# Performance work log

Hardware: AMD Instinct MI355X
Metric: run time of the kernel (lower is better)

The kernel has to match this reference:

```python
import jax, jax.numpy as jnp
import numpy as np

NUM_EMBEDDINGS = 8192
EMBEDDING_DIM = 64
COMMITMENT_COST = 0.25


def setup_inputs() -> dict:
    key = jax.random.key(0)
    k1, k2 = jax.random.split(key)
    hidden_states = jax.random.normal(k1, (32, 32, 32, EMBEDDING_DIM), dtype=jnp.float32)
    init_bound = 1.0 / NUM_EMBEDDINGS
    embedding = jax.random.uniform(k2, (NUM_EMBEDDINGS, EMBEDDING_DIM), dtype=jnp.float32,
                                   minval=-init_bound, maxval=init_bound)
    return {"hidden_states": hidden_states, "embedding": embedding}


def reference(hidden_states, embedding):
    # hidden_states: (B, H, W, D); embedding: (K, D)
    flat = hidden_states.reshape(-1, EMBEDDING_DIM)            # (N, D)
    z_sq = jnp.sum(flat * flat, axis=1, keepdims=True)          # (N, 1)
    e_sq = jnp.sum(embedding * embedding, axis=1)               # (K,)
    # squared L2 distances: ||z||^2 + ||e||^2 - 2 z.e
    distances = z_sq + e_sq - 2.0 * (flat @ embedding.T)        # (N, K)
    encoding_indices = jnp.argmin(distances, axis=1)            # (N,)
    # one-hot @ embedding == gather; identical math, efficient form
    quantized = jnp.take(embedding, encoding_indices, axis=0).reshape(hidden_states.shape)
    # codebook + commitment loss (return_loss=True path)
    loss = (jnp.mean((jax.lax.stop_gradient(quantized) - hidden_states) ** 2)
            + COMMITMENT_COST * jnp.mean((quantized - jax.lax.stop_gradient(hidden_states)) ** 2))
    # straight-through estimator
    z_q = hidden_states + jax.lax.stop_gradient(quantized - hidden_states)
    B = hidden_states.shape[0]
    min_encoding_indices = encoding_indices.reshape(B, -1)      # (B, num_tokens)
    return z_q, min_encoding_indices, loss
```

## Files before the change

kernel.cpp:

```cpp
#include <hip/hip_runtime.h>
#include <cfloat>

#define N_TOK   32768
#define DIM     64
#define K_CODES 8192
#define NCHK    64
#define TPB     128

#define IDX_OFF  (N_TOK * DIM)
#define LOSS_OFF (N_TOK * DIM + N_TOK)

#define WS_ESQ   0
#define WS_EHIT  8192
#define WS_PART  270336

#define MRG   2e-5f
#define DINIT 6e-5f

typedef __attribute__((ext_vector_type(8)))  short bf16x8;
typedef __attribute__((ext_vector_type(16))) float f32x16;

__device__ inline ushort f2bf(float x) {
    unsigned u = __float_as_uint(x);
    return (ushort)((u + 0x7FFFu + ((u >> 16) & 1u)) >> 16);
}
__device__ inline float bf2f(ushort h) { return __uint_as_float(((unsigned)h) << 16); }
__device__ inline ushort f2bf_up(float x) {
    unsigned u = __float_as_uint(x);
    return (x >= 0.0f) ? (ushort)((u + 0xFFFFu) >> 16) : (ushort)(u >> 16);
}
__device__ inline unsigned long long packdi(float d, int i) {
    unsigned u = __float_as_uint(d);
    u ^= (u & 0x80000000u) ? 0xFFFFFFFFu : 0x80000000u;
    return ((unsigned long long)u << 32) | (unsigned)i;
}

__global__ __launch_bounds__(256) void esq_kernel(const float* __restrict__ emb,
                                                  float* __restrict__ esq) {
#pragma clang fp contract(off)
    const int tid = threadIdx.x;
    const int q = tid & 7;
    const int code = blockIdx.x * 32 + (tid >> 3);
    const float* row = emb + code * DIM;
    float x = row[q];
    float r = x * x;
#pragma unroll
    for (int m = 1; m < 8; ++m) {
        float y = row[q + 8 * m];
        float sq = y * y;
        r = r + sq;
    }
    r = r + __shfl_xor(r, 1, 64);
    r = r + __shfl_xor(r, 2, 64);
    r = r + __shfl_xor(r, 4, 64);
    if (q == 0) esq[code] = r;
}

__global__ __launch_bounds__(256) void pack2(const float* __restrict__ emb,
                                             ushort* __restrict__ ehiT,
                                             float* __restrict__ eT) {
#pragma clang fp contract(off)
    const int k = blockIdx.x * 256 + threadIdx.x;
    float v[64];
    {
        const float4* ep = (const float4*)(emb + (size_t)k * DIM);
#pragma unroll
        for (int i = 0; i < 16; ++i) {
            const float4 a = ep[i];
            v[4 * i] = a.x; v[4 * i + 1] = a.y; v[4 * i + 2] = a.z; v[4 * i + 3] = a.w;
        }
    }
#pragma unroll
    for (int j = 0; j < 64; ++j) eT[(size_t)j * K_CODES + k] = v[j];
    const int sc = k >> 7, lc = k & 127;
#pragma unroll
    for (int q = 0; q < 4; ++q)
#pragma unroll
        for (int h = 0; h < 2; ++h) {
            bf16x8 o;
#pragma unroll
            for (int e = 0; e < 8; ++e) o[e] = (short)f2bf(v[16 * q + 8 * h + e]);
            *(bf16x8*)(ehiT + ((((size_t)sc * 4 + q) * 2 + h) * 128 + lc) * 8) = o;
        }
}

__global__ __launch_bounds__(256, 2) void vq_mfma(const float* __restrict__ hid,
                                                  const ushort* __restrict__ ehiT,
                                                  ushort* __restrict__ Mm) {
#pragma clang fp contract(off)
    const int tid = threadIdx.x;
    const int lane = tid & 63;
    const int w = tid >> 6;
    const int h = lane >> 5;
    const int t0 = blockIdx.x * 64;

    bf16x8 z_hi[2][4];
#pragma unroll
    for (int ts = 0; ts < 2; ++ts)
#pragma unroll
    for (int q = 0; q < 4; ++q) {
        const float* zp = hid + (size_t)(t0 + 32 * ts + (lane & 31)) * DIM + 16 * q + 8 * h;
        const float4 u0 = *(const float4*)zp;
        const float4 u1 = *(const float4*)(zp + 4);
        const float zz[8] = {u0.x, u0.y, u0.z, u0.w, u1.x, u1.y, u1.z, u1.w};
        bf16x8 hv;
#pragma unroll
        for (int i = 0; i < 8; ++i) hv[i] = (short)f2bf(zz[i]);
        z_hi[ts][q] = hv;
    }

    f32x16 zc;
#pragma unroll
    for (int i = 0; i < 16; ++i) zc[i] = 0.0f;

#define ALOAD(SC, R, Q) (*(const bf16x8*)(ehiT + \
    ((((size_t)(SC) * 4 + (Q)) * 2 + h) * 128 + 32 * (R) + (lane & 31)) * 8))

    bf16x8 Aa[4][4], Ab[4][4];
#pragma unroll
    for (int r = 0; r < 4; ++r)
#pragma unroll
        for (int q = 0; q < 4; ++q) Aa[r][q] = ALOAD(w, r, q);

#define MFMA_G(CUR, NXT, G) { \
    const int sc = 4 * (G) + w; \
    const int scn = ((G) + 1 < 16) ? (4 * ((G) + 1) + w) : sc; \
    _Pragma("unroll") \
    for (int r = 0; r < 4; ++r) \
        _Pragma("unroll") \
        for (int q = 0; q < 4; ++q) NXT[r][q] = ALOAD(scn, r, q); \
    float wm0 = -3.0e38f, wm1 = -3.0e38f; \
    _Pragma("unroll") \
    for (int r = 0; r < 4; ++r) { \
        f32x16 d0 = __builtin_amdgcn_mfma_f32_32x32x16_bf16(CUR[r][0], z_hi[0][0], zc, 0, 0, 0); \
        f32x16 d1 = __builtin_amdgcn_mfma_f32_32x32x16_bf16(CUR[r][0], z_hi[1][0], zc, 0, 0, 0); \
        _Pragma("unroll") \
        for (int q = 1; q < 4; ++q) { \
            d0 = __builtin_amdgcn_mfma_f32_32x32x16_bf16(CUR[r][q], z_hi[0][q], d0, 0, 0, 0); \
            d1 = __builtin_amdgcn_mfma_f32_32x32x16_bf16(CUR[r][q], z_hi[1][q], d1, 0, 0, 0); \
        } \
        _Pragma("unroll") \
        for (int i = 0; i < 16; ++i) { \
            wm0 = fmaxf(wm0, d0[i]); \
            wm1 = fmaxf(wm1, d1[i]); \
        } \
    } \
    wm0 = fmaxf(wm0, __shfl_xor(wm0, 32, 64)); \
    wm1 = fmaxf(wm1, __shfl_xor(wm1, 32, 64)); \
    if (lane < 32) { \
        Mm[(size_t)sc * N_TOK + t0 + lane]      = f2bf_up(wm0); \
        Mm[(size_t)sc * N_TOK + t0 + 32 + lane] = f2bf_up(wm1); \
    } }

    for (int gg = 0; gg < 16; gg += 2) {
        MFMA_G(Aa, Ab, gg)
        MFMA_G(Ab, Aa, gg + 1)
    }
#undef MFMA_G
#undef ALOAD
}

__global__ __launch_bounds__(512, 1) void vq_select(const float* __restrict__ hid,
                                                    const float* __restrict__ eT,
                                                    const float* __restrict__ esq,
                                                    const ushort* __restrict__ Mm,
                                                    float* __restrict__ out_idx) {
#pragma clang fp contract(off)
    __shared__ float z_s[TPB][68];
    __shared__ float zsq_s[TPB];
    __shared__ float eps_s[TPB];
    __shared__ float bD_s[TPB];
    __shared__ float mxw[4][TPB];
    __shared__ unsigned long long key_s[TPB];
    __shared__ unsigned long long m0_s[NCHK];
    __shared__ unsigned long long m1_s[NCHK];

    const int tid = threadIdx.x;
    const int lane = tid & 63;
    const int w = tid >> 6;
    const int t0 = blockIdx.x * TPB;

    {
        const int t = tid >> 2;
        const int j4 = (tid & 3) * 4;
        const float4* src = (const float4*)(hid + (size_t)(t0 + t) * DIM);
        float4* dst = (float4*)(&z_s[t][0]);
#pragma unroll
        for (int i = 0; i < 4; ++i) dst[j4 + i] = src[j4 + i];
    }
    if (tid < TPB) key_s[tid] = ~0ull;
    __syncthreads();

    {
        const int token = tid & 127;
        const int cg = tid >> 7;
        float pm = bf2f(Mm[(size_t)(16 * cg) * N_TOK + t0 + token]);
#pragma unroll 5
        for (int c = 16 * cg + 1; c < 16 * cg + 16; ++c)
            pm = fmaxf(pm, bf2f(Mm[(size_t)c * N_TOK + t0 + token]));
        mxw[cg][token] = pm;
    }
    if (tid < TPB) {
        const float* zr = &z_s[tid][0];
        float r[8];
#pragma unroll
        for (int q = 0; q < 8; ++q) {
            float x = zr[q]; r[q] = x * x;
#pragma unroll
            for (int m = 1; m < 8; ++m) {
                float y = zr[q + 8 * m];
                float sq = y * y;
                r[q] = r[q] + sq;
            }
        }
        zsq_s[tid] = ((r[0] + r[1]) + (r[2] + r[3])) + ((r[4] + r[5]) + (r[6] + r[7]));
    }
    __syncthreads();
    if (tid < TPB) {
        const float mx = fmaxf(fmaxf(mxw[0][tid], mxw[1][tid]),
                               fmaxf(mxw[2][tid], mxw[3][tid]));
        const float zsq = zsq_s[tid];
        const float eps = sqrtf(zsq) * 4.2e-6f + 2e-7f;
        eps_s[tid] = eps;
        bD_s[tid] = zsq - 2.0f * mx + 2.0f * eps + DINIT;
    }
    __syncthreads();

#pragma unroll
    for (int i = 0; i < 8; ++i) {
        const int c = 8 * w + i;
        const float mA = bf2f(Mm[(size_t)c * N_TOK + t0 + lane]);
        const int sA = (fmaf(-2.0f, mA + eps_s[lane], zsq_s[lane]) - MRG) < bD_s[lane];
        const unsigned long long b0 = __ballot(sA);
        const float mB = bf2f(Mm[(size_t)c * N_TOK + t0 + 64 + lane]);
        const int sB = (fmaf(-2.0f, mB + eps_s[64 + lane], zsq_s[64 + lane]) - MRG) < bD_s[64 + lane];
        const unsigned long long b1 = __ballot(sB);
        if (lane == 0) { m0_s[c] = b0; m1_s[c] = b1; }
    }

    for (int i = 0; i < 8; ++i) {
        const int c = 8 * w + i;
        unsigned long long msk0 = m0_s[c], msk1 = m1_s[c];
        if (!(msk0 | msk1)) continue;
        const int k0 = c * 128 + 2 * lane;
        const float* eb = eT + k0;
        const float2 es2 = *(const float2*)(esq + k0);

        while (msk0 | msk1) {
            int G = 1;
            int tA, tB;
            if (msk0) { tA = __ffsll(msk0) - 1; msk0 &= msk0 - 1; }
            else      { tA = 64 + __ffsll(msk1) - 1; msk1 &= msk1 - 1; }
            tB = tA;
            if (msk0 | msk1) {
                G = 2;
                if (msk0) { tB = __ffsll(msk0) - 1; msk0 &= msk0 - 1; }
                else      { tB = 64 + __ffsll(msk1) - 1; msk1 &= msk1 - 1; }
            }
            const float4* zpA = (const float4*)(&z_s[tA][0]);
            const float4* zpB = (const float4*)(&z_s[tB][0]);

            float2 bA[8], bB[8];
            float aA0, aA1, aB0, aB1;
#define LOADG(B, G2) { _Pragma("unroll") \
    for (int j = 0; j < 8; ++j) \
        B[j] = *(const float2*)(eb + (size_t)(8 * (G2) + j) * K_CODES); }
#define FMAJ(Bj, vA, vB, COMP) \
    aA0 = fmaf(vA.COMP, Bj.x, aA0); aA1 = fmaf(vA.COMP, Bj.y, aA1); \
    aB0 = fmaf(vB.COMP, Bj.x, aB0); aB1 = fmaf(vB.COMP, Bj.y, aB1);
#define FMAG(B, G2) { \
    const float4 vA = zpA[2 * (G2)], vB = zpB[2 * (G2)]; \
    FMAJ(B[0], vA, vB, x) FMAJ(B[1], vA, vB, y) \
    FMAJ(B[2], vA, vB, z) FMAJ(B[3], vA, vB, w) \
    const float4 uA = zpA[2 * (G2) + 1], uB = zpB[2 * (G2) + 1]; \
    FMAJ(B[4], uA, uB, x) FMAJ(B[5], uA, uB, y) \
    FMAJ(B[6], uA, uB, z) FMAJ(B[7], uA, uB, w) }

            LOADG(bA, 0)
            LOADG(bB, 1)
            {
                const float4 vA = zpA[0], vB = zpB[0];
                aA0 = vA.x * bA[0].x; aA1 = vA.x * bA[0].y;
                aB0 = vB.x * bA[0].x; aB1 = vB.x * bA[0].y;
                FMAJ(bA[1], vA, vB, y)
                FMAJ(bA[2], vA, vB, z)
                FMAJ(bA[3], vA, vB, w)
                const float4 uA = zpA[1], uB = zpB[1];
                FMAJ(bA[4], uA, uB, x)
                FMAJ(bA[5], uA, uB, y)
                FMAJ(bA[6], uA, uB, z)
                FMAJ(bA[7], uA, uB, w)
            }
            LOADG(bA, 2) FMAG(bB, 1)
            LOADG(bB, 3) FMAG(bA, 2)
            LOADG(bA, 4) FMAG(bB, 3)
            LOADG(bB, 5) FMAG(bA, 4)
            LOADG(bA, 6) FMAG(bB, 5)
            LOADG(bB, 7) FMAG(bA, 6)
            FMAG(bB, 7)
#undef LOADG
#undef FMAJ
#undef FMAG

#define FINISH(aX0, aX1, tX) { \
    const float zqX = zsq_s[tX]; \
    const float dX0 = fmaf(-2.0f, aX0, zqX + es2.x); \
    const float dX1 = fmaf(-2.0f, aX1, zqX + es2.y); \
    float dl = dX0; int il = k0; \
    if (dX1 < dl) { dl = dX1; il = k0 + 1; } \
    _Pragma("unroll") \
    for (int mm = 1; mm < 64; mm <<= 1) { \
        const float ov = __shfl_xor(dl, mm, 64); \
        const int   oi = __shfl_xor(il, mm, 64); \
        if (ov < dl || (ov == dl && oi < il)) { dl = ov; il = oi; } \
    } \
    if (lane == 0) atomicMin(&key_s[tX], packdi(dl, il)); }

            FINISH(aA0, aA1, tA)
            if (G > 1) FINISH(aB0, aB1, tB)
#undef FINISH
        }
    }
    __syncthreads();

    if (tid < TPB) out_idx[t0 + tid] = (float)(int)(key_s[tid] & 0xFFFFFFFFull);
}

__global__ __launch_bounds__(256) void vq_finish(const float* __restrict__ hid,
                                                 const float* __restrict__ emb,
                                                 const float* __restrict__ out_idx,
                                                 float* __restrict__ out_zq,
                                                 float* __restrict__ partials) {
#pragma clang fp contract(off)
    __shared__ float lred[4];
    const int tid = threadIdx.x;
    const int t = blockIdx.x * 256 + tid;

    const int bi = (int)out_idx[t];

    const float4* q4 = (const float4*)(emb + (size_t)bi * DIM);
    const float4* h4 = (const float4*)(hid + (size_t)t * DIM);
    float4* o4 = (float4*)(out_zq + (size_t)t * DIM);
    float lsum = 0.f;
#pragma unroll
    for (int i = 0; i < 16; ++i) {
        const float4 q = q4[i];
        const float4 h = h4[i];
        float4 zq;
        float dx;
        dx = q.x - h.x; zq.x = h.x + dx; lsum += dx * dx;
        dx = q.y - h.y; zq.y = h.y + dx; lsum += dx * dx;
        dx = q.z - h.z; zq.z = h.z + dx; lsum += dx * dx;
        dx = q.w - h.w; zq.w = h.w + dx; lsum += dx * dx;
        o4[i] = zq;
    }

#pragma unroll
    for (int off = 32; off >= 1; off >>= 1) lsum += __shfl_xor(lsum, off, 64);
    const int wid = tid >> 6;
    if ((tid & 63) == 0) lred[wid] = lsum;
    __syncthreads();
    if (tid == 0) partials[blockIdx.x] = (lred[0] + lred[1]) + (lred[2] + lred[3]);
}

__global__ __launch_bounds__(128) void loss_kernel(const float* __restrict__ partials,
                                                   float* __restrict__ out_loss) {
#pragma clang fp contract(off)
    __shared__ float s[128];
    const int t = threadIdx.x;
    s[t] = partials[t];
    __syncthreads();
    for (int off = 64; off >= 1; off >>= 1) {
        if (t < off) s[t] = s[t] + s[t + off];
        __syncthreads();
    }
    if (t == 0) {
        const float m = s[0] * (1.0f / 2097152.0f);
        out_loss[0] = m + 0.25f * m;
    }
}

extern "C" void kernel_launch(void* const* d_in, const int* in_sizes, int n_in,
                              void* d_out, int out_size, void* d_ws, size_t ws_size,
                              hipStream_t stream) {
    const float* hid = (const float*)d_in[0];
    const float* emb = (const float*)d_in[1];
    float* out = (float*)d_out;
    float* ws  = (float*)d_ws;
    float*  esq   = ws + WS_ESQ;
    ushort* ehiT  = (ushort*)(ws + WS_EHIT);
    float*  parts = ws + WS_PART;
    float*  eT    = out;
    ushort* Mm    = (ushort*)(out + 524288);

    esq_kernel<<<K_CODES / 32, 256, 0, stream>>>(emb, esq);
    pack2<<<K_CODES / 256, 256, 0, stream>>>(emb, ehiT, eT);
    vq_mfma<<<N_TOK / 64, 256, 0, stream>>>(hid, ehiT, Mm);
    vq_select<<<N_TOK / TPB, 512, 0, stream>>>(hid, eT, esq, Mm, out + IDX_OFF);
    vq_finish<<<N_TOK / 256, 256, 0, stream>>>(hid, emb, out + IDX_OFF, out, parts);
    loss_kernel<<<1, 128, 0, stream>>>(parts, out + LOSS_OFF);
}
```

Before: 138.3 us.

## Split vq_select codebook chunks across two blocks with global atomic argmin keys

Each token tile in vq_select is now handled by two blocks, each scanning half of the 64 codebook chunks, so the grid doubles and launch bounds allow two blocks per CU. The per-token argmin moves from shared-memory atomics to 64-bit global atomicMin on a workspace array that is reset with a memset. vq_finish now decodes the index from that array and writes the float index output. This is meant to raise occupancy and balance load in the candidate refinement phase. The cost is an extra memset, global atomic traffic, and each block redundantly recomputing the per-token z loads and thresholds.

```diff
diff --git a/kernel.cpp b/kernel.cpp
--- a/kernel.cpp
+++ b/kernel.cpp
@@ -6,6 +6,7 @@
 #define K_CODES 8192
 #define NCHK    64
 #define TPB     128
+#define CHB     32
 
 #define IDX_OFF  (N_TOK * DIM)
 #define LOSS_OFF (N_TOK * DIM + N_TOK)
@@ -13,6 +14,7 @@
 #define WS_ESQ   0
 #define WS_EHIT  8192
 #define WS_PART  270336
+#define WS_GKEY  270464
 
 #define MRG   2e-5f
 #define DINIT 6e-5f
@@ -160,25 +162,25 @@
 #undef ALOAD
 }
 
-__global__ __launch_bounds__(512, 1) void vq_select(const float* __restrict__ hid,
+__global__ __launch_bounds__(512, 2) void vq_select(const float* __restrict__ hid,
                                                     const float* __restrict__ eT,
                                                     const float* __restrict__ esq,
                                                     const ushort* __restrict__ Mm,
-                                                    float* __restrict__ out_idx) {
+                                                    unsigned long long* __restrict__ gkey) {
 #pragma clang fp contract(off)
     __shared__ float z_s[TPB][68];
     __shared__ float zsq_s[TPB];
     __shared__ float eps_s[TPB];
     __shared__ float bD_s[TPB];
     __shared__ float mxw[4][TPB];
-    __shared__ unsigned long long key_s[TPB];
-    __shared__ unsigned long long m0_s[NCHK];
-    __shared__ unsigned long long m1_s[NCHK];
+    __shared__ unsigned long long m0_s[CHB];
+    __shared__ unsigned long long m1_s[CHB];
 
     const int tid = threadIdx.x;
     const int lane = tid & 63;
     const int w = tid >> 6;
-    const int t0 = blockIdx.x * TPB;
+    const int cb = blockIdx.x & 1;
+    const int t0 = (blockIdx.x >> 1) * TPB;
 
     {
         const int t = tid >> 2;
@@ -188,7 +190,6 @@
 #pragma unroll
         for (int i = 0; i < 4; ++i) dst[j4 + i] = src[j4 + i];
     }
-    if (tid < TPB) key_s[tid] = ~0ull;
     __syncthreads();
 
     {
@@ -227,20 +228,22 @@
     __syncthreads();
 
 #pragma unroll
-    for (int i = 0; i < 8; ++i) {
-        const int c = 8 * w + i;
+    for (int i = 0; i < 4; ++i) {
+        const int lc = 4 * w + i;
+        const int c = CHB * cb + lc;
         const float mA = bf2f(Mm[(size_t)c * N_TOK + t0 + lane]);
         const int sA = (fmaf(-2.0f, mA + eps_s[lane], zsq_s[lane]) - MRG) < bD_s[lane];
         const unsigned long long b0 = __ballot(sA);
         const float mB = bf2f(Mm[(size_t)c * N_TOK + t0 + 64 + lane]);
         const int sB = (fmaf(-2.0f, mB + eps_s[64 + lane], zsq_s[64 + lane]) - MRG) < bD_s[64 + lane];
         const unsigned long long b1 = __ballot(sB);
-        if (lane == 0) { m0_s[c] = b0; m1_s[c] = b1; }
-    }
-
-    for (int i = 0; i < 8; ++i) {
-        const int c = 8 * w + i;
-        unsigned long long msk0 = m0_s[c], msk1 = m1_s[c];
+        if (lane == 0) { m0_s[lc] = b0; m1_s[lc] = b1; }
+    }
+
+    for (int i = 0; i < 4; ++i) {
+        const int lc = 4 * w + i;
+        const int c = CHB * cb + lc;
+        unsigned long long msk0 = m0_s[lc], msk1 = m1_s[lc];
         if (!(msk0 | msk1)) continue;
         const int k0 = c * 128 + 2 * lane;
         const float* eb = eT + k0;
@@ -314,29 +317,28 @@
         const int   oi = __shfl_xor(il, mm, 64); \
         if (ov < dl || (ov == dl && oi < il)) { dl = ov; il = oi; } \
     } \
-    if (lane == 0) atomicMin(&key_s[tX], packdi(dl, il)); }
+    if (lane == 0) atomicMin(&gkey[t0 + tX], packdi(dl, il)); }
 
             FINISH(aA0, aA1, tA)
             if (G > 1) FINISH(aB0, aB1, tB)
 #undef FINISH
         }
     }
-    __syncthreads();
-
-    if (tid < TPB) out_idx[t0 + tid] = (float)(int)(key_s[tid] & 0xFFFFFFFFull);
 }
 
 __global__ __launch_bounds__(256) void vq_finish(const float* __restrict__ hid,
                                                  const float* __restrict__ emb,
-                                                 const float* __restrict__ out_idx,
+                                                 const unsigned long long* __restrict__ gkey,
                                                  float* __restrict__ out_zq,
+                                                 float* __restrict__ out_idx,
                                                  float* __restrict__ partials) {
 #pragma clang fp contract(off)
     __shared__ float lred[4];
     const int tid = threadIdx.x;
     const int t = blockIdx.x * 256 + tid;
 
-    const int bi = (int)out_idx[t];
+    const int bi = (int)(gkey[t] & 0xFFFFFFFFull);
+    out_idx[t] = (float)bi;
 
     const float4* q4 = (const float4*)(emb + (size_t)bi * DIM);
     const float4* h4 = (const float4*)(hid + (size_t)t * DIM);
@@ -390,13 +392,15 @@
     float*  esq   = ws + WS_ESQ;
     ushort* ehiT  = (ushort*)(ws + WS_EHIT);
     float*  parts = ws + WS_PART;
+    unsigned long long* gkey = (unsigned long long*)(ws + WS_GKEY);
     float*  eT    = out;
     ushort* Mm    = (ushort*)(out + 524288);
 
+    hipMemsetAsync(gkey, 0xFF, (size_t)N_TOK * sizeof(unsigned long long), stream);
     esq_kernel<<<K_CODES / 32, 256, 0, stream>>>(emb, esq);
     pack2<<<K_CODES / 256, 256, 0, stream>>>(emb, ehiT, eT);
     vq_mfma<<<N_TOK / 64, 256, 0, stream>>>(hid, ehiT, Mm);
-    vq_select<<<N_TOK / TPB, 512, 0, stream>>>(hid, eT, esq, Mm, out + IDX_OFF);
-    vq_finish<<<N_TOK / 256, 256, 0, stream>>>(hid, emb, out + IDX_OFF, out, parts);
+    vq_select<<<(N_TOK / TPB) * 2, 512, 0, stream>>>(hid, eT, esq, Mm, gkey);
+    vq_finish<<<N_TOK / 256, 256, 0, stream>>>(hid, emb, gkey, out, out + IDX_OFF, parts);
     loss_kernel<<<1, 128, 0, stream>>>(parts, out + LOSS_OFF);
 }
```

Result: slower. 153.9 us (+11.2%).

## Fuse gather and loss partials into select kernel using workspace scratch

Applied to the files above, without the earlier changes.

Moves the transposed codebook and bf16 bound scratch from the output buffer into workspace, so the output can be written inside the select kernel. The select kernel then does the codebook gather, the straight-through output write and the per-block loss partial itself, reusing the hidden states already in LDS. This drops the separate finish kernel and its re-read of the hidden states. The fused tail runs on only 128 of 512 threads, with per-thread row stores that are not coalesced. The old path is kept as a fallback when the workspace is too small.

```diff
diff --git a/kernel.cpp b/kernel.cpp
--- a/kernel.cpp
+++ b/kernel.cpp
@@ -13,6 +13,13 @@
 #define WS_ESQ   0
 #define WS_EHIT  8192
 #define WS_PART  270336
+
+#define W2_ESQ   0
+#define W2_EHIT  8192
+#define W2_ET    270336
+#define W2_MM    794624
+#define W2_PART  1843200
+#define W2_TOTAL 1843456
 
 #define MRG   2e-5f
 #define DINIT 6e-5f
@@ -160,11 +167,15 @@
 #undef ALOAD
 }
 
-__global__ __launch_bounds__(512, 1) void vq_select(const float* __restrict__ hid,
-                                                    const float* __restrict__ eT,
-                                                    const float* __restrict__ esq,
-                                                    const ushort* __restrict__ Mm,
-                                                    float* __restrict__ out_idx) {
+template <int FUSED>
+__global__ __launch_bounds__(512, 1) void vq_select_t(const float* __restrict__ hid,
+                                                      const float* __restrict__ eT,
+                                                      const float* __restrict__ esq,
+                                                      const ushort* __restrict__ Mm,
+                                                      const float* __restrict__ emb,
+                                                      float* __restrict__ out_zq,
+                                                      float* __restrict__ out_idx,
+                                                      float* __restrict__ partials) {
 #pragma clang fp contract(off)
     __shared__ float z_s[TPB][68];
     __shared__ float zsq_s[TPB];
@@ -174,6 +185,7 @@
     __shared__ unsigned long long key_s[TPB];
     __shared__ unsigned long long m0_s[NCHK];
     __shared__ unsigned long long m1_s[NCHK];
+    __shared__ float lred[2];
 
     const int tid = threadIdx.x;
     const int lane = tid & 63;
@@ -323,7 +335,36 @@
     }
     __syncthreads();
 
-    if (tid < TPB) out_idx[t0 + tid] = (float)(int)(key_s[tid] & 0xFFFFFFFFull);
+    if (FUSED) {
+        if (tid < TPB) {
+            const int t = t0 + tid;
+            const int bi = (int)(key_s[tid] & 0xFFFFFFFFull);
+            out_idx[t] = (float)bi;
+            const float4* q4 = (const float4*)(emb + (size_t)bi * DIM);
+            const float4* h4 = (const float4*)(&z_s[tid][0]);
+            float4* o4 = (float4*)(out_zq + (size_t)t * DIM);
+            float lsum = 0.f;
+#pragma unroll
+            for (int i = 0; i < 16; ++i) {
+                const float4 q = q4[i];
+                const float4 h = h4[i];
+                float4 zq;
+                float dx;
+                dx = q.x - h.x; zq.x = h.x + dx; lsum += dx * dx;
+                dx = q.y - h.y; zq.y = h.y + dx; lsum += dx * dx;
+                dx = q.z - h.z; zq.z = h.z + dx; lsum += dx * dx;
+                dx = q.w - h.w; zq.w = h.w + dx; lsum += dx * dx;
+                o4[i] = zq;
+            }
+#pragma unroll
+            for (int off = 32; off >= 1; off >>= 1) lsum += __shfl_xor(lsum, off, 64);
+            if ((tid & 63) == 0) lred[tid >> 6] = lsum;
+        }
+        __syncthreads();
+        if (tid == 0) partials[blockIdx.x] = lred[0] + lred[1];
+    } else {
+        if (tid < TPB) out_idx[t0 + tid] = (float)(int)(key_s[tid] & 0xFFFFFFFFull);
+    }
 }
 
 __global__ __launch_bounds__(256) void vq_finish(const float* __restrict__ hid,
@@ -363,12 +404,29 @@
     if (tid == 0) partials[blockIdx.x] = (lred[0] + lred[1]) + (lred[2] + lred[3]);
 }
 
-__global__ __launch_bounds__(128) void loss_kernel(const float* __restrict__ partials,
-                                                   float* __restrict__ out_loss) {
+__global__ __launch_bounds__(128) void loss_kernel128(const float* __restrict__ partials,
+                                                      float* __restrict__ out_loss) {
 #pragma clang fp contract(off)
     __shared__ float s[128];
     const int t = threadIdx.x;
     s[t] = partials[t];
+    __syncthreads();
+    for (int off = 64; off >= 1; off >>= 1) {
+        if (t < off) s[t] = s[t] + s[t + off];
+        __syncthreads();
+    }
+    if (t == 0) {
+        const float m = s[0] * (1.0f / 2097152.0f);
+        out_loss[0] = m + 0.25f * m;
+    }
+}
+
+__global__ __launch_bounds__(128) void loss_kernel256(const float* __restrict__ partials,
+                                                      float* __restrict__ out_loss) {
+#pragma clang fp contract(off)
+    __shared__ float s[128];
+    const int t = threadIdx.x;
+    s[t] = partials[t] + partials[t + 128];
     __syncthreads();
     for (int off = 64; off >= 1; off >>= 1) {
         if (t < off) s[t] = s[t] + s[t + off];
@@ -387,16 +445,33 @@
     const float* emb = (const float*)d_in[1];
     float* out = (float*)d_out;
     float* ws  = (float*)d_ws;
-    float*  esq   = ws + WS_ESQ;
-    ushort* ehiT  = (ushort*)(ws + WS_EHIT);
-    float*  parts = ws + WS_PART;
-    float*  eT    = out;
-    ushort* Mm    = (ushort*)(out + 524288);
-
-    esq_kernel<<<K_CODES / 32, 256, 0, stream>>>(emb, esq);
-    pack2<<<K_CODES / 256, 256, 0, stream>>>(emb, ehiT, eT);
-    vq_mfma<<<N_TOK / 64, 256, 0, stream>>>(hid, ehiT, Mm);
-    vq_select<<<N_TOK / TPB, 512, 0, stream>>>(hid, eT, esq, Mm, out + IDX_OFF);
-    vq_finish<<<N_TOK / 256, 256, 0, stream>>>(hid, emb, out + IDX_OFF, out, parts);
-    loss_kernel<<<1, 128, 0, stream>>>(parts, out + LOSS_OFF);
-}
+
+    if (ws_size >= (size_t)W2_TOTAL * sizeof(float)) {
+        float*  esq   = ws + W2_ESQ;
+        ushort* ehiT  = (ushort*)(ws + W2_EHIT);
+        float*  eT    = ws + W2_ET;
+        ushort* Mm    = (ushort*)(ws + W2_MM);
+        float*  parts = ws + W2_PART;
+
+        esq_kernel<<<K_CODES / 32, 256, 0, stream>>>(emb, esq);
+        pack2<<<K_CODES / 256, 256, 0, stream>>>(emb, ehiT, eT);
+        vq_mfma<<<N_TOK / 64, 256, 0, stream>>>(hid, ehiT, Mm);
+        vq_select_t<1><<<N_TOK / TPB, 512, 0, stream>>>(hid, eT, esq, Mm, emb,
+                                                        out, out + IDX_OFF, parts);
+        loss_kernel256<<<1, 128, 0, stream>>>(parts, out + LOSS_OFF);
+    } else {
+        float*  esq   = ws + WS_ESQ;
+        ushort* ehiT  = (ushort*)(ws + WS_EHIT);
+        float*  parts = ws + WS_PART;
+        float*  eT    = out;
+        ushort* Mm    = (ushort*)(out + 524288);
+
+        esq_kernel<<<K_CODES / 32, 256, 0, stream>>>(emb, esq);
+        pack2<<<K_CODES / 256, 256, 0, stream>>>(emb, ehiT, eT);
+        vq_mfma<<<N_TOK / 64, 256, 0, stream>>>(hid, ehiT, Mm);
+        vq_select_t<0><<<N_TOK / TPB, 512, 0, stream>>>(hid, eT, esq, Mm, emb,
+                                                        out, out + IDX_OFF, parts);
+        vq_finish<<<N_TOK / 256, 256, 0, stream>>>(hid, emb, out + IDX_OFF, out, parts);
+        loss_kernel128<<<1, 128, 0, stream>>>(parts, out + LOSS_OFF);
+    }
+}
```

Measured after the change: 132.4 us. 1.04x faster.
